# Performance work log

Measured on AMD Instinct MI355X. Metric: run time of the kernel, lower is better.

Reference implementation:

```python
import jax, jax.numpy as jnp
import numpy as np

H = 256
W = 256
N = 10000
CHUNK = 500  # N must be divisible by CHUNK
CHOL_BOUND = np.array([0.5, 0.0, 0.5], dtype=np.float32)  # cholesky_bound buffer


def setup_inputs() -> dict:
    key = jax.random.key(0)
    k1, k2, k3 = jax.random.split(key, 3)
    xyz = jax.random.normal(k1, (N, 2), dtype=jnp.float32)          # atanh-space positions
    cholesky = jax.random.uniform(k2, (N, 3), dtype=jnp.float32)    # lower-tri elems (pre-bound)
    colors = jax.random.normal(k3, (N, 3), dtype=jnp.float32)       # _colors (used raw)
    opacity = jnp.ones((N, 1), dtype=jnp.float32)                   # _opacity buffer
    scale_factor = jnp.asarray(1.0, dtype=jnp.float32)
    shift_factor = jnp.asarray(0.0, dtype=jnp.float32)
    return {"xyz": xyz, "cholesky": cholesky, "colors": colors,
            "opacity": opacity, "scale_factor": scale_factor, "shift_factor": shift_factor}


def _render(xyz, cholesky, colors, opacity, scale_factor, shift_factor):
    # --- project_gaussians_2d ---
    means = jnp.tanh(xyz)                                   # map to (-1, 1)
    cx = 0.5 * W * (means[:, 0] + 1.0)                      # pixel-space centers (N,)
    cy = 0.5 * H * (means[:, 1] + 1.0)
    L = cholesky + jnp.asarray(CHOL_BOUND)                  # get_cholesky_elements
    cov_xx = L[:, 0] * L[:, 0]
    cov_xy = L[:, 0] * L[:, 1]
    cov_yy = L[:, 1] * L[:, 1] + L[:, 2] * L[:, 2]
    det = cov_xx * cov_yy - cov_xy * cov_xy
    conic_a = cov_yy / det                                  # inverse covariance (conic)
    conic_b = -cov_xy / det
    conic_c = cov_xx / det
    op = opacity[:, 0]

    px = jnp.arange(W, dtype=jnp.float32)[None, :]          # (1, W) pixel x coords
    py = jnp.arange(H, dtype=jnp.float32)[:, None]          # (H, 1) pixel y coords

    def resh(v):
        return v.reshape((N // CHUNK, CHUNK) + v.shape[1:])

    stacked = jax.tree.map(resh, (cx, cy, conic_a, conic_b, conic_c, op, colors))

    # --- rasterize_gaussians_sum: out[h,w,:] = sum_n alpha_n(h,w) * color_n ---
    def body(acc, xs):
        cxc, cyc, ac, bc, cc, oc, colc = xs
        dx = cxc[:, None, None] - px[None]                  # (C, 1, W)
        dy = cyc[:, None, None] - py[None]                  # (C, H, 1)
        sigma = (0.5 * (ac[:, None, None] * dx * dx + cc[:, None, None] * dy * dy)
                 + bc[:, None, None] * (dx * dy))           # (C, H, W)
        alpha = oc[:, None, None] * jnp.exp(-sigma)
        alpha = jnp.where((sigma >= 0.0) & (alpha >= 1.0 / 255.0),
                          jnp.minimum(alpha, 0.999), 0.0)
        acc = acc + jnp.einsum('nhw,nc->hwc', alpha, colc)
        return acc, None

    img, _ = jax.lax.scan(body, jnp.zeros((H, W, 3), dtype=jnp.float32), stacked)
    img = img * scale_factor + shift_factor
    return jnp.transpose(img, (2, 0, 1))                    # (3, H, W)


def reference(xyz, cholesky, colors, opacity, scale_factor, shift_factor):
    return _render(xyz, cholesky, colors, opacity, scale_factor, shift_factor)
```

## Files before the change

### kernel.cpp

```cpp
#include <hip/hip_runtime.h>


#define IMG_H 256
#define IMG_W 256
#define TILE 8
#define TPX 32
#define NTILES 1024
#define CAP 512
#define CSTRIDE 16

__global__ __launch_bounds__(64) void prep_bin_kernel(
    const float* __restrict__ xyz,
    const float* __restrict__ chol,
    const float* __restrict__ colors,
    const float* __restrict__ opacity,
    int N,
    int* __restrict__ counts,
    int* __restrict__ lists,
    float4* __restrict__ params)
{
    const int n = blockIdx.x * 64 + threadIdx.x;
    if (n >= N) return;

    const float mx = tanhf(xyz[2 * n + 0]);
    const float my = tanhf(xyz[2 * n + 1]);
    const float cx = 0.5f * IMG_W * (mx + 1.0f);
    const float cy = 0.5f * IMG_H * (my + 1.0f);

    const float L0 = chol[3 * n + 0] + 0.5f;
    const float L1 = chol[3 * n + 1];
    const float L2 = chol[3 * n + 2] + 0.5f;
    const float cov_xx = L0 * L0;
    const float cov_xy = L0 * L1;
    const float cov_yy = L1 * L1 + L2 * L2;
    const float det = cov_xx * cov_yy - cov_xy * cov_xy;

    const float conic_a = cov_yy / det;
    const float conic_b = -cov_xy / det;
    const float conic_c = cov_xx / det;
    const float op = opacity[n];

    params[3 * n + 0] = make_float4(cx, cy, conic_a, conic_b);
    params[3 * n + 1] = make_float4(conic_c, op, colors[3 * n + 0], colors[3 * n + 1]);
    params[3 * n + 2] = make_float4(colors[3 * n + 2], 0.0f, 0.0f, 0.0f);

    const float smax = logf(255.0f * op);
    if (!(smax > 0.0f)) return;

    const float rx = sqrtf(2.0f * smax * cov_xx) + 1.0f;
    const float ry = sqrtf(2.0f * smax * cov_yy) + 1.0f;
    const int x0 = max(0, (int)floorf(cx - rx));
    const int x1 = min(IMG_W - 1, (int)ceilf(cx + rx));
    const int y0 = max(0, (int)floorf(cy - ry));
    const int y1 = min(IMG_H - 1, (int)ceilf(cy + ry));
    if (x0 > x1 || y0 > y1) return;

    const int tx0 = x0 >> 3, tx1 = x1 >> 3;
    const int ty0 = y0 >> 3, ty1 = y1 >> 3;
    for (int ty = ty0; ty <= ty1; ++ty) {
        for (int tx = tx0; tx <= tx1; ++tx) {
            const int t = ty * TPX + tx;
            const int slot = atomicAdd(&counts[t * CSTRIDE], 1);
            if (slot < CAP) lists[t * CAP + slot] = n;
        }
    }
}

__global__ __launch_bounds__(256) void render_kernel(
    const int* __restrict__ counts,
    const int* __restrict__ lists,
    const float4* __restrict__ params,
    const float* __restrict__ scale,
    const float* __restrict__ shift,
    float* __restrict__ out)
{
    const int tile = blockIdx.x;
    const int tx = tile & (TPX - 1);
    const int ty = tile >> 5;
    const int wave = threadIdx.x >> 6;
    const int p = threadIdx.x & 63;
    const float px = (float)(tx * TILE + (p & (TILE - 1)));
    const float py = (float)(ty * TILE + (p >> 3));

    __shared__ float4 sh[3 * 256];
    __shared__ float red[3][256];

    const int cnt = min(counts[tile * CSTRIDE], CAP);
    const int* list = lists + tile * CAP;

    float accr = 0.0f, accg = 0.0f, accb = 0.0f;

    for (int base = 0; base < cnt; base += 256) {
        const int m = min(256, cnt - base);
        __syncthreads();
        if (threadIdx.x < m) {
            const int n = list[base + threadIdx.x];
            sh[3 * threadIdx.x + 0] = params[3 * n + 0];
            sh[3 * threadIdx.x + 1] = params[3 * n + 1];
            sh[3 * threadIdx.x + 2] = params[3 * n + 2];
        }
        __syncthreads();
        for (int j = wave; j < m; j += 4) {
            const float4 p0 = sh[3 * j + 0];
            const float4 p1 = sh[3 * j + 1];
            const float c2v = sh[3 * j + 2].x;
            const float dx = p0.x - px;
            const float dy = p0.y - py;
            const float sigma =
                0.5f * (p0.z * dx * dx + p1.x * dy * dy) + p0.w * (dx * dy);
            float alpha = p1.y * __expf(-sigma);
            if (sigma >= 0.0f && alpha >= (1.0f / 255.0f)) {
                alpha = fminf(alpha, 0.999f);
                accr = fmaf(alpha, p1.z, accr);
                accg = fmaf(alpha, p1.w, accg);
                accb = fmaf(alpha, c2v, accb);
            }
        }
    }

    red[0][threadIdx.x] = accr;
    red[1][threadIdx.x] = accg;
    red[2][threadIdx.x] = accb;
    __syncthreads();

    if (threadIdx.x < 192) {
        const int c = threadIdx.x >> 6;
        const int q = threadIdx.x & 63;
        const float sum = red[c][q] + red[c][q + 64] + red[c][q + 128] + red[c][q + 192];
        const int pix = (ty * TILE + (q >> 3)) * IMG_W + tx * TILE + (q & (TILE - 1));
        out[c * IMG_H * IMG_W + pix] = fmaf(sum, scale[0], shift[0]);
    }
}

extern "C" void kernel_launch(void* const* d_in, const int* in_sizes, int n_in,
                              void* d_out, int out_size, void* d_ws, size_t ws_size,
                              hipStream_t stream) {
    const float* xyz     = (const float*)d_in[0];
    const float* chol    = (const float*)d_in[1];
    const float* colors  = (const float*)d_in[2];
    const float* opacity = (const float*)d_in[3];
    const float* scale   = (const float*)d_in[4];
    const float* shift   = (const float*)d_in[5];
    float* out = (float*)d_out;

    const int N = in_sizes[3];

    int* counts = (int*)d_ws;
    int* lists = counts + NTILES * CSTRIDE;
    float4* params = (float4*)(lists + NTILES * CAP);

    hipMemsetAsync(counts, 0, NTILES * CSTRIDE * sizeof(int), stream);
    prep_bin_kernel<<<(N + 63) / 64, 64, 0, stream>>>(
        xyz, chol, colors, opacity, N, counts, lists, params);
    render_kernel<<<NTILES, 256, 0, stream>>>(counts, lists, params, scale, shift, out);
}
```

Before: 76.41 us.

## Replace global atomic binning with per-tile bbox scan in shared memory

The prep kernel now writes a packed tile-space bounding box per Gaussian instead of appending indices to per-tile global lists with global atomics. Each render block scans all N bboxes, compacts the matching indices into a shared-memory list using wave ballots and a shared atomic, then rasterizes as before. This removes the memset, the contended global atomics and the scattered list writes, but every one of the 1024 blocks now reads all N bbox words. The order of indices within a tile list also changes, which may alter the floating-point summation order.

```diff
diff --git a/kernel.cpp b/kernel.cpp
--- a/kernel.cpp
+++ b/kernel.cpp
@@ -7,19 +7,17 @@
 #define TPX 32
 #define NTILES 1024
 #define CAP 512
-#define CSTRIDE 16
 
-__global__ __launch_bounds__(64) void prep_bin_kernel(
+__global__ __launch_bounds__(256) void prep_kernel(
     const float* __restrict__ xyz,
     const float* __restrict__ chol,
     const float* __restrict__ colors,
     const float* __restrict__ opacity,
     int N,
-    int* __restrict__ counts,
-    int* __restrict__ lists,
+    unsigned int* __restrict__ bbox,
     float4* __restrict__ params)
 {
-    const int n = blockIdx.x * 64 + threadIdx.x;
+    const int n = blockIdx.x * 256 + threadIdx.x;
     if (n >= N) return;
 
     const float mx = tanhf(xyz[2 * n + 0]);
@@ -35,66 +33,79 @@
     const float cov_yy = L1 * L1 + L2 * L2;
     const float det = cov_xx * cov_yy - cov_xy * cov_xy;
 
-    const float conic_a = cov_yy / det;
-    const float conic_b = -cov_xy / det;
-    const float conic_c = cov_xx / det;
-    const float op = opacity[n];
-
-    params[3 * n + 0] = make_float4(cx, cy, conic_a, conic_b);
-    params[3 * n + 1] = make_float4(conic_c, op, colors[3 * n + 0], colors[3 * n + 1]);
+    params[3 * n + 0] = make_float4(cx, cy, cov_yy / det, -cov_xy / det);
+    params[3 * n + 1] = make_float4(cov_xx / det, opacity[n],
+                                    colors[3 * n + 0], colors[3 * n + 1]);
     params[3 * n + 2] = make_float4(colors[3 * n + 2], 0.0f, 0.0f, 0.0f);
 
-    const float smax = logf(255.0f * op);
-    if (!(smax > 0.0f)) return;
-
-    const float rx = sqrtf(2.0f * smax * cov_xx) + 1.0f;
-    const float ry = sqrtf(2.0f * smax * cov_yy) + 1.0f;
-    const int x0 = max(0, (int)floorf(cx - rx));
-    const int x1 = min(IMG_W - 1, (int)ceilf(cx + rx));
-    const int y0 = max(0, (int)floorf(cy - ry));
-    const int y1 = min(IMG_H - 1, (int)ceilf(cy + ry));
-    if (x0 > x1 || y0 > y1) return;
-
-    const int tx0 = x0 >> 3, tx1 = x1 >> 3;
-    const int ty0 = y0 >> 3, ty1 = y1 >> 3;
-    for (int ty = ty0; ty <= ty1; ++ty) {
-        for (int tx = tx0; tx <= tx1; ++tx) {
-            const int t = ty * TPX + tx;
-            const int slot = atomicAdd(&counts[t * CSTRIDE], 1);
-            if (slot < CAP) lists[t * CAP + slot] = n;
+    const float smax = logf(255.0f * opacity[n]);
+    unsigned int packed = 0xFFFFFFFFu;
+    if (smax > 0.0f) {
+        const float rx = sqrtf(2.0f * smax * cov_xx) + 1.0f;
+        const float ry = sqrtf(2.0f * smax * cov_yy) + 1.0f;
+        const int x0 = max(0, (int)floorf(cx - rx));
+        const int x1 = min(IMG_W - 1, (int)ceilf(cx + rx));
+        const int y0 = max(0, (int)floorf(cy - ry));
+        const int y1 = min(IMG_H - 1, (int)ceilf(cy + ry));
+        if (x0 <= x1 && y0 <= y1) {
+            packed = (unsigned int)(x0 >> 3) | ((unsigned int)(x1 >> 3) << 5) |
+                     ((unsigned int)(y0 >> 3) << 10) | ((unsigned int)(y1 >> 3) << 15);
         }
     }
+    bbox[n] = packed;
 }
 
 __global__ __launch_bounds__(256) void render_kernel(
-    const int* __restrict__ counts,
-    const int* __restrict__ lists,
+    const unsigned int* __restrict__ bbox,
     const float4* __restrict__ params,
     const float* __restrict__ scale,
     const float* __restrict__ shift,
+    int N,
     float* __restrict__ out)
 {
     const int tile = blockIdx.x;
     const int tx = tile & (TPX - 1);
     const int ty = tile >> 5;
     const int wave = threadIdx.x >> 6;
-    const int p = threadIdx.x & 63;
+    const int lane = threadIdx.x & 63;
+    const int p = lane;
     const float px = (float)(tx * TILE + (p & (TILE - 1)));
     const float py = (float)(ty * TILE + (p >> 3));
 
+    __shared__ int lcnt;
+    __shared__ int lidx[CAP];
     __shared__ float4 sh[3 * 256];
     __shared__ float red[3][256];
 
-    const int cnt = min(counts[tile * CSTRIDE], CAP);
-    const int* list = lists + tile * CAP;
+    if (threadIdx.x == 0) lcnt = 0;
+    __syncthreads();
+
+    const unsigned int txu = (unsigned int)tx;
+    const unsigned int tyu = (unsigned int)ty;
+    for (int i = threadIdx.x; i < N; i += 256) {
+        const unsigned int b = bbox[i];
+        const bool match = ((b & 31u) <= txu) && (txu <= ((b >> 5) & 31u)) &&
+                           (((b >> 10) & 31u) <= tyu) && (tyu <= ((b >> 15) & 31u));
+        const unsigned long long mask = __ballot(match);
+        if (match) {
+            const int leader = __ffsll((long long)mask) - 1;
+            const int pos = __popcll(mask & ((1ull << lane) - 1ull));
+            int basep = 0;
+            if (lane == leader) basep = atomicAdd(&lcnt, __popcll(mask));
+            basep = __shfl(basep, leader);
+            const int slot = basep + pos;
+            if (slot < CAP) lidx[slot] = i;
+        }
+    }
+    __syncthreads();
+    const int cnt = min(lcnt, CAP);
 
     float accr = 0.0f, accg = 0.0f, accb = 0.0f;
 
     for (int base = 0; base < cnt; base += 256) {
         const int m = min(256, cnt - base);
-        __syncthreads();
         if (threadIdx.x < m) {
-            const int n = list[base + threadIdx.x];
+            const int n = lidx[base + threadIdx.x];
             sh[3 * threadIdx.x + 0] = params[3 * n + 0];
             sh[3 * threadIdx.x + 1] = params[3 * n + 1];
             sh[3 * threadIdx.x + 2] = params[3 * n + 2];
@@ -116,6 +127,7 @@
                 accb = fmaf(alpha, c2v, accb);
             }
         }
+        __syncthreads();
     }
 
     red[0][threadIdx.x] = accr;
@@ -145,12 +157,10 @@
 
     const int N = in_sizes[3];
 
-    int* counts = (int*)d_ws;
-    int* lists = counts + NTILES * CSTRIDE;
-    float4* params = (float4*)(lists + NTILES * CAP);
+    unsigned int* bbox = (unsigned int*)d_ws;
+    float4* params = (float4*)((char*)d_ws + ((N * 4 + 15) & ~15));
 
-    hipMemsetAsync(counts, 0, NTILES * CSTRIDE * sizeof(int), stream);
-    prep_bin_kernel<<<(N + 63) / 64, 64, 0, stream>>>(
-        xyz, chol, colors, opacity, N, counts, lists, params);
-    render_kernel<<<NTILES, 256, 0, stream>>>(counts, lists, params, scale, shift, out);
+    prep_kernel<<<(N + 255) / 256, 256, 0, stream>>>(
+        xyz, chol, colors, opacity, N, bbox, params);
+    render_kernel<<<NTILES, 256, 0, stream>>>(bbox, params, scale, shift, N, out);
 }
```

Result: slower. 83.89 us (+9.8%).
